# Performance work log

Measured on AMD Instinct MI355X. Metric: run time of the kernel, lower is better.

## Reference

```python
import jax, jax.numpy as jnp
import numpy as np

DIM = 768
HEADS = 12
HEAD_DIM = DIM // HEADS
HIDDEN = int(DIM * 4.0)
EPS = 1e-5


def layernorm(x, w, b):
    mu = jnp.mean(x, axis=-1, keepdims=True)
    var = jnp.var(x, axis=-1, keepdims=True)
    return (x - mu) * jax.lax.rsqrt(var + EPS) * w + b


def setup_inputs() -> dict:
    key = jax.random.key(0)
    ks = jax.random.split(key, 12)
    B, N = 4, 2048
    s = lambda fan_in: 1.0 / np.sqrt(fan_in)
    return {
        "x": jax.random.normal(ks[0], (B, N, DIM), dtype=jnp.float32),
        "qkv_w": jax.random.normal(ks[1], (3 * DIM, DIM), dtype=jnp.float32) * s(DIM),
        "proj_w": jax.random.normal(ks[2], (DIM, DIM), dtype=jnp.float32) * s(DIM),
        "proj_b": jnp.zeros((DIM,), dtype=jnp.float32),
        "norm1_w": jnp.ones((DIM,), dtype=jnp.float32),
        "norm1_b": jnp.zeros((DIM,), dtype=jnp.float32),
        "norm2_w": jnp.ones((DIM,), dtype=jnp.float32),
        "norm2_b": jnp.zeros((DIM,), dtype=jnp.float32),
        "fc1_w": jax.random.normal(ks[3], (HIDDEN, DIM), dtype=jnp.float32) * s(DIM),
        "fc1_b": jnp.zeros((HIDDEN,), dtype=jnp.float32),
        "fc2_w": jax.random.normal(ks[4], (DIM, HIDDEN), dtype=jnp.float32) * s(HIDDEN),
        "fc2_b": jnp.zeros((DIM,), dtype=jnp.float32),
    }


def reference(x, qkv_w, proj_w, proj_b, norm1_w, norm1_b, norm2_w, norm2_b,
              fc1_w, fc1_b, fc2_w, fc2_b):
    B, N, C = x.shape
    scale = HEAD_DIM ** -0.5
    shortcut = x
    h = layernorm(x, norm1_w, norm1_b)
    # qkv: [B, N, 3C] -> [3, B, H, N, Dh]
    qkv = (h @ qkv_w.T).reshape(B, N, 3, HEADS, HEAD_DIM)
    qkv = jnp.transpose(qkv, (2, 0, 3, 1, 4))
    q, k, v = qkv[0] * scale, qkv[1], qkv[2]
    attn = jnp.einsum("bhnd,bhmd->bhnm", q, k)
    attn = jax.nn.softmax(attn, axis=-1)
    out = jnp.einsum("bhnm,bhmd->bhnd", attn, v)
    out = jnp.transpose(out, (0, 2, 1, 3)).reshape(B, N, C)
    out = out @ proj_w.T + proj_b
    x = shortcut + out
    h2 = layernorm(x, norm2_w, norm2_b)
    mlp = jax.nn.gelu(h2 @ fc1_w.T + fc1_b, approximate=False) @ fc2_w.T + fc2_b
    return x + mlp
```

## Files before the change

### kernel.cpp

```cpp
#include <hip/hip_runtime.h>
#include <hip/hip_bf16.h>

#define SEQ   2048
#define NBAT  4
#define NH    12
#define HD    64
#define CDIM  768
#define HID   3072
#define NTOK  (SEQ*NBAT)

#define KS2 0.1803368801111244f

typedef __attribute__((ext_vector_type(8))) short short8;
typedef __attribute__((ext_vector_type(4))) float floatx4;

__device__ __forceinline__ float bf2f(unsigned short u) {
    union { unsigned int i; float f; } v; v.i = ((unsigned int)u) << 16; return v.f;
}
__device__ __forceinline__ unsigned short f2bf(float f) {
    union { float f; unsigned int i; } v; v.f = f;
    unsigned int i = v.i;
    return (unsigned short)((i + 0x7FFFu + ((i >> 16) & 1u)) >> 16);
}
__device__ __forceinline__ unsigned int fbits(float f) {
    union { float f; unsigned int i; } v; v.f = f; return v.i;
}
__device__ __forceinline__ float fast_exp2(float x) {
#if __has_builtin(__builtin_amdgcn_exp2f)
    return __builtin_amdgcn_exp2f(x);
#else
    return __expf(x * 0.69314718055994531f);
#endif
}
__device__ __forceinline__ float fast_rcp(float x) {
#if __has_builtin(__builtin_amdgcn_rcpf)
    return __builtin_amdgcn_rcpf(x);
#else
    return 1.f / x;
#endif
}
__device__ __forceinline__ float gelu_f(float v) {
    float u = 0.7978845608028654f * v * (1.f + 0.044715f * v * v);
    float e = fast_exp2(u * 2.885390081777927f);
    float th = 1.f - 2.f * fast_rcp(e + 1.f);
    return 0.5f * v * (1.f + th);
}
__device__ __forceinline__ void gload16(const unsigned short* g, unsigned short* l) {
    __builtin_amdgcn_global_load_lds(
        (const __attribute__((address_space(1))) unsigned int*)g,
        (__attribute__((address_space(3))) unsigned int*)l, 16, 0, 0);
}
__device__ __forceinline__ void pl32_swap(unsigned int& x, unsigned int& y) {
    asm("v_permlane32_swap_b32 %0, %1" : "+v"(x), "+v"(y));
}
__device__ __forceinline__ void pl16_swap(unsigned int& x, unsigned int& y) {
    asm("v_permlane16_swap_b32 %0, %1" : "+v"(x), "+v"(y));
}

__global__ __launch_bounds__(256) void cvt_all_kernel(
    const float* __restrict__ s0, const float* __restrict__ s1,
    const float* __restrict__ s2, const float* __restrict__ s3,
    unsigned short* __restrict__ d0, unsigned short* __restrict__ d1,
    unsigned short* __restrict__ d2, unsigned short* __restrict__ d3)
{
    int blk = blockIdx.x;
    const float* src; unsigned short* dst; int off;
    if (blk < 1728)      { src = s0; dst = d0; off = blk; }
    else if (blk < 2304) { src = s1; dst = d1; off = blk - 1728; }
    else if (blk < 4608) { src = s2; dst = d2; off = blk - 2304; }
    else                 { src = s3; dst = d3; off = blk - 4608; }
    int i = (off * 256 + threadIdx.x) * 4;
    float4 f = *(const float4*)(src + i);
    ushort4 o;
    o.x = f2bf(f.x); o.y = f2bf(f.y); o.z = f2bf(f.z); o.w = f2bf(f.w);
    *(ushort4*)(dst + i) = o;
}

__global__ __launch_bounds__(256) void ln_kernel(
    const float* __restrict__ x, const float* __restrict__ w,
    const float* __restrict__ b, unsigned short* __restrict__ y)
{
    int row  = blockIdx.x * 4 + (threadIdx.x >> 6);
    int lane = threadIdx.x & 63;
    const float4* xr = (const float4*)(x + (size_t)row * CDIM);
    float4 v[3];
    float s = 0.f, sq = 0.f;
#pragma unroll
    for (int i = 0; i < 3; i++) {
        float4 f = xr[lane + i * 64];
        v[i] = f;
        s  += (f.x + f.y) + (f.z + f.w);
        sq += (f.x * f.x + f.y * f.y) + (f.z * f.z + f.w * f.w);
    }
#pragma unroll
    for (int o = 32; o > 0; o >>= 1) {
        s  += __shfl_xor(s,  o, 64);
        sq += __shfl_xor(sq, o, 64);
    }
    float mean = s * (1.f / CDIM);
    float var  = sq * (1.f / CDIM) - mean * mean;
    float rstd = rsqrtf(var + 1e-5f);
    const float4* w4 = (const float4*)w;
    const float4* b4 = (const float4*)b;
    ushort4* y4 = (ushort4*)(y + (size_t)row * CDIM);
#pragma unroll
    for (int i = 0; i < 3; i++) {
        int c = lane + i * 64;
        float4 wf = w4[c], bf_ = b4[c];
        ushort4 o;
        o.x = f2bf((v[i].x - mean) * rstd * wf.x + bf_.x);
        o.y = f2bf((v[i].y - mean) * rstd * wf.y + bf_.y);
        o.z = f2bf((v[i].z - mean) * rstd * wf.z + bf_.z);
        o.w = f2bf((v[i].w - mean) * rstd * wf.w + bf_.w);
        y4[c] = o;
    }
}

#define BK 64

template<int ACT, int OUT32, int TM, int DBUF>
__global__ __launch_bounds__(256) void gemm_bt(
    const unsigned short* __restrict__ A, const unsigned short* __restrict__ W,
    const float* __restrict__ bias, const float* __restrict__ res,
    void* __restrict__ Cv, int M, int N, int K, int scol, float scale)
{
    constexpr int MT   = TM / 32;
    constexpr int ISSA = TM / 32;
    constexpr int NB   = DBUF ? 2 : 1;
    __shared__ __align__(16) unsigned short As[NB * TM * BK];
    __shared__ __align__(16) unsigned short Bs[NB * 128 * BK];
    int tid  = threadIdx.x;
    int wave = tid >> 6, lane = tid & 63;
    int wr = wave >> 1, wc = wave & 1;
    int quad = lane >> 4, l15 = lane & 15;
    int m0 = blockIdx.x * TM, n0 = blockIdx.y * 128;

    int r8 = lane >> 3;
    int kc = (lane & 7) ^ r8;
    const unsigned short* Ag = A + (size_t)(m0 + wave * (TM / 4) + r8) * K + kc * 8;
    const unsigned short* Wg = W + (size_t)(n0 + wave * 32 + r8) * K + kc * 8;
    unsigned short* AsW = As + wave * (TM / 4) * BK;
    unsigned short* BsW = Bs + wave * 32 * BK;

    floatx4 acc[MT][4];
    floatx4 fz = {0.f, 0.f, 0.f, 0.f};
#pragma unroll
    for (int i = 0; i < MT; i++)
#pragma unroll
        for (int j = 0; j < 4; j++) acc[i][j] = fz;

    int sw = l15 & 7;

    if constexpr (DBUF == 0) {
        for (int k0 = 0; k0 < K; k0 += BK) {
            __syncthreads();
#pragma unroll
            for (int j = 0; j < ISSA; j++)
                gload16(Ag + (size_t)(8 * j) * K + k0, AsW + j * 512);
#pragma unroll
            for (int j = 0; j < 4; j++)
                gload16(Wg + (size_t)(8 * j) * K + k0, BsW + j * 512);
            __syncthreads();

#pragma unroll
            for (int s = 0; s < 2; s++) {
                short8 af[MT], bfg[4];
                int ko = ((s * 4 + quad) ^ sw) * 8;
#pragma unroll
                for (int mt = 0; mt < MT; mt++)
                    af[mt] = *(const short8*)(As + (wr * (TM / 2) + mt * 16 + l15) * BK + ko);
#pragma unroll
                for (int nt = 0; nt < 4; nt++)
                    bfg[nt] = *(const short8*)(Bs + (wc * 64 + nt * 16 + l15) * BK + ko);
#pragma unroll
                for (int mt = 0; mt < MT; mt++)
#pragma unroll
                    for (int nt = 0; nt < 4; nt++)
                        acc[mt][nt] = __builtin_amdgcn_mfma_f32_16x16x32_bf16(
                            af[mt], bfg[nt], acc[mt][nt], 0, 0, 0);
            }
        }
    } else {
#pragma unroll
        for (int j = 0; j < ISSA; j++)
            gload16(Ag + (size_t)(8 * j) * K, AsW + j * 512);
#pragma unroll
        for (int j = 0; j < 4; j++)
            gload16(Wg + (size_t)(8 * j) * K, BsW + j * 512);
        int cur = 0;
        for (int k0 = 0; k0 < K; k0 += BK) {
            __syncthreads();
            if (k0 + BK < K) {
                int nb = cur ^ 1;
#pragma unroll
                for (int j = 0; j < ISSA; j++)
                    gload16(Ag + (size_t)(8 * j) * K + k0 + BK, AsW + nb * (TM * BK) + j * 512);
#pragma unroll
                for (int j = 0; j < 4; j++)
                    gload16(Wg + (size_t)(8 * j) * K + k0 + BK, BsW + nb * (128 * BK) + j * 512);
            }
            const unsigned short* Asb = As + cur * (TM * BK);
            const unsigned short* Bsb = Bs + cur * (128 * BK);
#pragma unroll
            for (int s = 0; s < 2; s++) {
                short8 af[MT], bfg[4];
                int ko = ((s * 4 + quad) ^ sw) * 8;
#pragma unroll
                for (int mt = 0; mt < MT; mt++)
                    af[mt] = *(const short8*)(Asb + (wr * (TM / 2) + mt * 16 + l15) * BK + ko);
#pragma unroll
                for (int nt = 0; nt < 4; nt++)
                    bfg[nt] = *(const short8*)(Bsb + (wc * 64 + nt * 16 + l15) * BK + ko);
#pragma unroll
                for (int mt = 0; mt < MT; mt++)
#pragma unroll
                    for (int nt = 0; nt < 4; nt++)
                        acc[mt][nt] = __builtin_amdgcn_mfma_f32_16x16x32_bf16(
                            af[mt], bfg[nt], acc[mt][nt], 0, 0, 0);
            }
            cur ^= 1;
        }
    }

#pragma unroll
    for (int mt = 0; mt < MT; mt++) {
#pragma unroll
        for (int nt = 0; nt < 4; nt++) {
            int col = n0 + wc * 64 + nt * 16 + l15;
            float bv = bias ? bias[col] : 0.f;
            float cs = (col < scol) ? scale : 1.f;
#pragma unroll
            for (int r = 0; r < 4; r++) {
                int row = m0 + wr * (TM / 2) + mt * 16 + quad * 4 + r;
                size_t idx = (size_t)row * N + col;
                float v = acc[mt][nt][r] + bv;
                if (res) v += res[idx];
                if (ACT == 1) v = gelu_f(v);
                v *= cs;
                if (OUT32) ((float*)Cv)[idx] = v;
                else       ((unsigned short*)Cv)[idx] = f2bf(v);
            }
        }
    }
}

__global__ __launch_bounds__(256, 4) void attn_kernel(
    const unsigned short* __restrict__ qkv, unsigned short* __restrict__ out)
{
    __shared__ __align__(16) unsigned short Ks[2][64 * 64];
    __shared__ __align__(16) unsigned short Vt[2][64 * 72];

    int tid  = threadIdx.x;
    int wave = tid >> 6, lane = tid & 63;
    int quad = lane >> 4, l15 = lane & 15;

    int f  = blockIdx.y * gridDim.x + blockIdx.x;
    int w_ = (f & 7) * 96 + (f >> 3);
    int qblk = w_ & 15;
    int bh   = w_ >> 4;
    int b  = bh / NH, h = bh % NH;
    size_t base = (size_t)b * SEQ * 2304 + h * 64;
    int qbase = qblk * 128 + wave * 32;

    short8 bq[2][2];
#pragma unroll
    for (int qh = 0; qh < 2; qh++)
#pragma unroll
        for (int kk = 0; kk < 2; kk++)
            bq[qh][kk] = *(const short8*)(qkv + base +
                (size_t)(qbase + qh * 16 + l15) * 2304 + kk * 32 + quad * 8);

    floatx4 o[2][4];
    floatx4 fz = {0.f, 0.f, 0.f, 0.f};
#pragma unroll
    for (int qh = 0; qh < 2; qh++)
#pragma unroll
        for (int dg = 0; dg < 4; dg++) o[qh][dg] = fz;
    float ls[2] = {0.f, 0.f};

    const unsigned short* kg = qkv + base + 768 +
        (size_t)(wave * 16 + (lane >> 3)) * 2304 + (((lane & 7) ^ ((lane >> 3) & 7)) * 8);
    const unsigned short* vptr = qkv + base + 1536;
    int vj  = tid & 31;
    int vd8 = wave * 16 + ((tid >> 5) & 1) * 8;
    int sw  = l15 & 7;

    gload16(kg, &Ks[0][wave * 1024]);
    gload16(kg + (size_t)8 * 2304, &Ks[0][wave * 1024 + 512]);
    {
        uint4 v0v = *(const uint4*)(vptr + (size_t)(2 * vj)     * 2304 + vd8);
        uint4 v1v = *(const uint4*)(vptr + (size_t)(2 * vj + 1) * 2304 + vd8);
        union { uint4 q; unsigned short u[8]; } u0, u1;
        u0.q = v0v; u1.q = v1v;
#pragma unroll
        for (int i = 0; i < 8; i++) {
            unsigned int w = (unsigned int)u0.u[i] | ((unsigned int)u1.u[i] << 16);
            *(unsigned int*)(&Vt[0][(vd8 + i) * 72 + 2 * vj]) = w;
        }
    }
    __syncthreads();

    for (int t = 0; t < SEQ / 64; t++) {
        int cur = t & 1, nxt = cur ^ 1;
        bool more = (t + 1 < SEQ / 64);
        uint4 v0v, v1v;
        if (more) {
            const unsigned short* kg2 = kg + (size_t)(t + 1) * 64 * 2304;
            gload16(kg2, &Ks[nxt][wave * 1024]);
            gload16(kg2 + (size_t)8 * 2304, &Ks[nxt][wave * 1024 + 512]);
            int kt = (t + 1) * 64;
            v0v = *(const uint4*)(vptr + (size_t)(kt + 2 * vj)     * 2304 + vd8);
            v1v = *(const uint4*)(vptr + (size_t)(kt + 2 * vj + 1) * 2304 + vd8);
        }

        floatx4 st[2][4];
        __builtin_amdgcn_s_setprio(1);
#pragma unroll
        for (int ts = 0; ts < 4; ts++) {
            short8 ak0 = *(const short8*)(&Ks[cur][(ts * 16 + l15) * 64 + (((0 * 4 + quad) ^ sw) * 8)]);
            short8 ak1 = *(const short8*)(&Ks[cur][(ts * 16 + l15) * 64 + (((1 * 4 + quad) ^ sw) * 8)]);
            floatx4 s0 = __builtin_amdgcn_mfma_f32_16x16x32_bf16(ak0, bq[0][0], fz, 0, 0, 0);
            s0 = __builtin_amdgcn_mfma_f32_16x16x32_bf16(ak1, bq[0][1], s0, 0, 0, 0);
            floatx4 s1 = __builtin_amdgcn_mfma_f32_16x16x32_bf16(ak0, bq[1][0], fz, 0, 0, 0);
            s1 = __builtin_amdgcn_mfma_f32_16x16x32_bf16(ak1, bq[1][1], s1, 0, 0, 0);
            st[0][ts] = s0; st[1][ts] = s1;
        }
        __builtin_amdgcn_s_setprio(0);

        unsigned int pw[2][4][2];
#pragma unroll
        for (int qh = 0; qh < 2; qh++) {
            float psum = 0.f;
#pragma unroll
            for (int ts = 0; ts < 4; ts++) {
                float p0 = fast_exp2(st[qh][ts][0]);
                float p1 = fast_exp2(st[qh][ts][1]);
                float p2 = fast_exp2(st[qh][ts][2]);
                float p3 = fast_exp2(st[qh][ts][3]);
                psum += (p0 + p1) + (p2 + p3);
                pw[qh][ts][0] = __builtin_amdgcn_perm(fbits(p1), fbits(p0), 0x07060302);
                pw[qh][ts][1] = __builtin_amdgcn_perm(fbits(p3), fbits(p2), 0x07060302);
            }
            ls[qh] += psum;
        }

#pragma unroll
        for (int hk = 0; hk < 2; hk++) {
            short8 bp[2];
#pragma unroll
            for (int qh = 0; qh < 2; qh++) {
                unsigned int x0 = pw[qh][2 * hk][0], y0 = pw[qh][2 * hk + 1][0];
                unsigned int x1 = pw[qh][2 * hk][1], y1 = pw[qh][2 * hk + 1][1];
                pl32_swap(x0, y0); pl16_swap(x0, y0);
                pl32_swap(x1, y1); pl16_swap(x1, y1);
                union { unsigned int u[4]; short8 s; } fu;
                fu.u[0] = x0; fu.u[1] = x1; fu.u[2] = y0; fu.u[3] = y1;
                bp[qh] = fu.s;
            }
            __builtin_amdgcn_s_setprio(1);
#pragma unroll
            for (int dg = 0; dg < 4; dg++) {
                short8 av = *(const short8*)(&Vt[cur][(dg * 16 + l15) * 72 + hk * 32 + quad * 8]);
                o[0][dg] = __builtin_amdgcn_mfma_f32_16x16x32_bf16(av, bp[0], o[0][dg], 0, 0, 0);
                o[1][dg] = __builtin_amdgcn_mfma_f32_16x16x32_bf16(av, bp[1], o[1][dg], 0, 0, 0);
            }
            __builtin_amdgcn_s_setprio(0);
        }

        if (more) {
            union { uint4 q; unsigned short u[8]; } u0, u1;
            u0.q = v0v; u1.q = v1v;
#pragma unroll
            for (int i = 0; i < 8; i++) {
                unsigned int w = (unsigned int)u0.u[i] | ((unsigned int)u1.u[i] << 16);
                *(unsigned int*)(&Vt[nxt][(vd8 + i) * 72 + 2 * vj]) = w;
            }
        }
        __syncthreads();
    }

#pragma unroll
    for (int qh = 0; qh < 2; qh++) {
        float l = ls[qh];
        l += __shfl_xor(l, 16, 64);
        l += __shfl_xor(l, 32, 64);
        float inv = 1.f / l;
        size_t orow = ((size_t)b * SEQ + qbase + qh * 16 + l15) * CDIM + h * 64;
#pragma unroll
        for (int dg = 0; dg < 4; dg++) {
            unsigned int u0 = (unsigned int)f2bf(o[qh][dg][0] * inv) | ((unsigned int)f2bf(o[qh][dg][1] * inv) << 16);
            unsigned int u1 = (unsigned int)f2bf(o[qh][dg][2] * inv) | ((unsigned int)f2bf(o[qh][dg][3] * inv) << 16);
            uint2 wv; wv.x = u0; wv.y = u1;
            *(uint2*)((unsigned short*)out + orow + dg * 16 + quad * 4) = wv;
        }
    }
}

extern "C" void kernel_launch(void* const* d_in, const int* in_sizes, int n_in,
                              void* d_out, int out_size, void* d_ws, size_t ws_size,
                              hipStream_t stream)
{
    const float* x      = (const float*)d_in[0];
    const float* qkv_w  = (const float*)d_in[1];
    const float* proj_w = (const float*)d_in[2];
    const float* proj_b = (const float*)d_in[3];
    const float* n1w    = (const float*)d_in[4];
    const float* n1b    = (const float*)d_in[5];
    const float* n2w    = (const float*)d_in[6];
    const float* n2b    = (const float*)d_in[7];
    const float* fc1w   = (const float*)d_in[8];
    const float* fc1b   = (const float*)d_in[9];
    const float* fc2w   = (const float*)d_in[10];
    const float* fc2b   = (const float*)d_in[11];
    float* out = (float*)d_out;

    unsigned short* ws = (unsigned short*)d_ws;
    unsigned short* wq = ws;
    unsigned short* wp = wq + 1769472;
    unsigned short* w1 = wp + 589824;
    unsigned short* w2 = w1 + 2359296;
    unsigned short* h    = w2 + 2359296;
    unsigned short* qkv  = h + 6291456;
    unsigned short* attn = qkv + 18874368;
    unsigned short* a    = qkv;

    dim3 blk(256);
    cvt_all_kernel<<<6912, blk, 0, stream>>>(qkv_w, proj_w, fc1w, fc2w, wq, wp, w1, w2);

    ln_kernel<<<NTOK / 4, blk, 0, stream>>>(x, n1w, n1b, h);
    gemm_bt<0, 0, 128, 0><<<dim3(NTOK / 128, 2304 / 128), blk, 0, stream>>>(
        h, wq, nullptr, nullptr, qkv, NTOK, 2304, 768, 768, KS2);
    attn_kernel<<<dim3(SEQ / 128, NBAT * NH), blk, 0, stream>>>(qkv, attn);
    gemm_bt<0, 1, 64, 1><<<dim3(NTOK / 64, 768 / 128), blk, 0, stream>>>(
        attn, wp, proj_b, x, out, NTOK, 768, 768, 0, 1.f);
    ln_kernel<<<NTOK / 4, blk, 0, stream>>>(out, n2w, n2b, h);
    gemm_bt<1, 0, 128, 0><<<dim3(NTOK / 128, 3072 / 128), blk, 0, stream>>>(
        h, w1, fc1b, nullptr, a, NTOK, 3072, 768, 0, 1.f);
    gemm_bt<0, 1, 64, 1><<<dim3(NTOK / 64, 768 / 128), blk, 0, stream>>>(
        a, w2, fc2b, out, out, NTOK, 768, 3072, 0, 1.f);
}
```

Before: 359.2 us.

## Split attention query block across eight waves of 16 rows each

After: 361.9 us, median of 2. No clear change (+0.7%).

```diff
diff --git a/kernel.cpp b/kernel.cpp
--- a/kernel.cpp
+++ b/kernel.cpp
@@ -244,7 +244,7 @@
     }
 }
 
-__global__ __launch_bounds__(256, 4) void attn_kernel(
+__global__ __launch_bounds__(512, 4) void attn_kernel(
     const unsigned short* __restrict__ qkv, unsigned short* __restrict__ out)
 {
     __shared__ __align__(16) unsigned short Ks[2][64 * 64];
@@ -260,34 +260,29 @@
     int bh   = w_ >> 4;
     int b  = bh / NH, h = bh % NH;
     size_t base = (size_t)b * SEQ * 2304 + h * 64;
-    int qbase = qblk * 128 + wave * 32;
-
-    short8 bq[2][2];
-#pragma unroll
-    for (int qh = 0; qh < 2; qh++)
-#pragma unroll
-        for (int kk = 0; kk < 2; kk++)
-            bq[qh][kk] = *(const short8*)(qkv + base +
-                (size_t)(qbase + qh * 16 + l15) * 2304 + kk * 32 + quad * 8);
-
-    floatx4 o[2][4];
+    int qbase = qblk * 128 + wave * 16;
+
+    short8 bq[2];
+#pragma unroll
+    for (int kk = 0; kk < 2; kk++)
+        bq[kk] = *(const short8*)(qkv + base +
+            (size_t)(qbase + l15) * 2304 + kk * 32 + quad * 8);
+
+    floatx4 o[4];
     floatx4 fz = {0.f, 0.f, 0.f, 0.f};
 #pragma unroll
-    for (int qh = 0; qh < 2; qh++)
-#pragma unroll
-        for (int dg = 0; dg < 4; dg++) o[qh][dg] = fz;
-    float ls[2] = {0.f, 0.f};
+    for (int dg = 0; dg < 4; dg++) o[dg] = fz;
+    float ls = 0.f;
 
     const unsigned short* kg = qkv + base + 768 +
-        (size_t)(wave * 16 + (lane >> 3)) * 2304 + (((lane & 7) ^ ((lane >> 3) & 7)) * 8);
+        (size_t)(wave * 8 + (lane >> 3)) * 2304 + (((lane & 7) ^ ((lane >> 3) & 7)) * 8);
     const unsigned short* vptr = qkv + base + 1536;
     int vj  = tid & 31;
     int vd8 = wave * 16 + ((tid >> 5) & 1) * 8;
     int sw  = l15 & 7;
 
-    gload16(kg, &Ks[0][wave * 1024]);
-    gload16(kg + (size_t)8 * 2304, &Ks[0][wave * 1024 + 512]);
-    {
+    gload16(kg, &Ks[0][wave * 512]);
+    if (wave < 4) {
         uint4 v0v = *(const uint4*)(vptr + (size_t)(2 * vj)     * 2304 + vd8);
         uint4 v1v = *(const uint4*)(vptr + (size_t)(2 * vj + 1) * 2304 + vd8);
         union { uint4 q; unsigned short u[8]; } u0, u1;
@@ -306,68 +301,61 @@
         uint4 v0v, v1v;
         if (more) {
             const unsigned short* kg2 = kg + (size_t)(t + 1) * 64 * 2304;
-            gload16(kg2, &Ks[nxt][wave * 1024]);
-            gload16(kg2 + (size_t)8 * 2304, &Ks[nxt][wave * 1024 + 512]);
-            int kt = (t + 1) * 64;
-            v0v = *(const uint4*)(vptr + (size_t)(kt + 2 * vj)     * 2304 + vd8);
-            v1v = *(const uint4*)(vptr + (size_t)(kt + 2 * vj + 1) * 2304 + vd8);
-        }
-
-        floatx4 st[2][4];
+            gload16(kg2, &Ks[nxt][wave * 512]);
+            if (wave < 4) {
+                int kt = (t + 1) * 64;
+                v0v = *(const uint4*)(vptr + (size_t)(kt + 2 * vj)     * 2304 + vd8);
+                v1v = *(const uint4*)(vptr + (size_t)(kt + 2 * vj + 1) * 2304 + vd8);
+            }
+        }
+
+        floatx4 st[4];
         __builtin_amdgcn_s_setprio(1);
 #pragma unroll
         for (int ts = 0; ts < 4; ts++) {
             short8 ak0 = *(const short8*)(&Ks[cur][(ts * 16 + l15) * 64 + (((0 * 4 + quad) ^ sw) * 8)]);
             short8 ak1 = *(const short8*)(&Ks[cur][(ts * 16 + l15) * 64 + (((1 * 4 + quad) ^ sw) * 8)]);
-            floatx4 s0 = __builtin_amdgcn_mfma_f32_16x16x32_bf16(ak0, bq[0][0], fz, 0, 0, 0);
-            s0 = __builtin_amdgcn_mfma_f32_16x16x32_bf16(ak1, bq[0][1], s0, 0, 0, 0);
-            floatx4 s1 = __builtin_amdgcn_mfma_f32_16x16x32_bf16(ak0, bq[1][0], fz, 0, 0, 0);
-            s1 = __builtin_amdgcn_mfma_f32_16x16x32_bf16(ak1, bq[1][1], s1, 0, 0, 0);
-            st[0][ts] = s0; st[1][ts] = s1;
+            floatx4 s0 = __builtin_amdgcn_mfma_f32_16x16x32_bf16(ak0, bq[0], fz, 0, 0, 0);
+            s0 = __builtin_amdgcn_mfma_f32_16x16x32_bf16(ak1, bq[1], s0, 0, 0, 0);
+            st[ts] = s0;
         }
         __builtin_amdgcn_s_setprio(0);
 
-        unsigned int pw[2][4][2];
-#pragma unroll
-        for (int qh = 0; qh < 2; qh++) {
+        unsigned int pw[4][2];
+        {
             float psum = 0.f;
 #pragma unroll
             for (int ts = 0; ts < 4; ts++) {
-                float p0 = fast_exp2(st[qh][ts][0]);
-                float p1 = fast_exp2(st[qh][ts][1]);
-                float p2 = fast_exp2(st[qh][ts][2]);
-                float p3 = fast_exp2(st[qh][ts][3]);
+                float p0 = fast_exp2(st[ts][0]);
+                float p1 = fast_exp2(st[ts][1]);
+                float p2 = fast_exp2(st[ts][2]);
+                float p3 = fast_exp2(st[ts][3]);
                 psum += (p0 + p1) + (p2 + p3);
-                pw[qh][ts][0] = __builtin_amdgcn_perm(fbits(p1), fbits(p0), 0x07060302);
-                pw[qh][ts][1] = __builtin_amdgcn_perm(fbits(p3), fbits(p2), 0x07060302);
-            }
-            ls[qh] += psum;
+                pw[ts][0] = __builtin_amdgcn_perm(fbits(p1), fbits(p0), 0x07060302);
+                pw[ts][1] = __builtin_amdgcn_perm(fbits(p3), fbits(p2), 0x07060302);
+            }
+            ls += psum;
         }
 
 #pragma unroll
         for (int hk = 0; hk < 2; hk++) {
-            short8 bp[2];
-#pragma unroll
-            for (int qh = 0; qh < 2; qh++) {
-                unsigned int x0 = pw[qh][2 * hk][0], y0 = pw[qh][2 * hk + 1][0];
-                unsigned int x1 = pw[qh][2 * hk][1], y1 = pw[qh][2 * hk + 1][1];
-                pl32_swap(x0, y0); pl16_swap(x0, y0);
-                pl32_swap(x1, y1); pl16_swap(x1, y1);
-                union { unsigned int u[4]; short8 s; } fu;
-                fu.u[0] = x0; fu.u[1] = x1; fu.u[2] = y0; fu.u[3] = y1;
-                bp[qh] = fu.s;
-            }
+            unsigned int x0 = pw[2 * hk][0], y0 = pw[2 * hk + 1][0];
+            unsigned int x1 = pw[2 * hk][1], y1 = pw[2 * hk + 1][1];
+            pl32_swap(x0, y0); pl16_swap(x0, y0);
+            pl32_swap(x1, y1); pl16_swap(x1, y1);
+            union { unsigned int u[4]; short8 s; } fu;
+            fu.u[0] = x0; fu.u[1] = x1; fu.u[2] = y0; fu.u[3] = y1;
+            short8 bp = fu.s;
             __builtin_amdgcn_s_setprio(1);
 #pragma unroll
             for (int dg = 0; dg < 4; dg++) {
                 short8 av = *(const short8*)(&Vt[cur][(dg * 16 + l15) * 72 + hk * 32 + quad * 8]);
-                o[0][dg] = __builtin_amdgcn_mfma_f32_16x16x32_bf16(av, bp[0], o[0][dg], 0, 0, 0);
-                o[1][dg] = __builtin_amdgcn_mfma_f32_16x16x32_bf16(av, bp[1], o[1][dg], 0, 0, 0);
+                o[dg] = __builtin_amdgcn_mfma_f32_16x16x32_bf16(av, bp, o[dg], 0, 0, 0);
             }
             __builtin_amdgcn_s_setprio(0);
         }
 
-        if (more) {
+        if (more && wave < 4) {
             union { uint4 q; unsigned short u[8]; } u0, u1;
             u0.q = v0v; u1.q = v1v;
 #pragma unroll
@@ -379,17 +367,16 @@
         __syncthreads();
     }
 
-#pragma unroll
-    for (int qh = 0; qh < 2; qh++) {
-        float l = ls[qh];
+    {
+        float l = ls;
         l += __shfl_xor(l, 16, 64);
         l += __shfl_xor(l, 32, 64);
         float inv = 1.f / l;
-        size_t orow = ((size_t)b * SEQ + qbase + qh * 16 + l15) * CDIM + h * 64;
+        size_t orow = ((size_t)b * SEQ + qbase + l15) * CDIM + h * 64;
 #pragma unroll
         for (int dg = 0; dg < 4; dg++) {
-            unsigned int u0 = (unsigned int)f2bf(o[qh][dg][0] * inv) | ((unsigned int)f2bf(o[qh][dg][1] * inv) << 16);
-            unsigned int u1 = (unsigned int)f2bf(o[qh][dg][2] * inv) | ((unsigned int)f2bf(o[qh][dg][3] * inv) << 16);
+            unsigned int u0 = (unsigned int)f2bf(o[dg][0] * inv) | ((unsigned int)f2bf(o[dg][1] * inv) << 16);
+            unsigned int u1 = (unsigned int)f2bf(o[dg][2] * inv) | ((unsigned int)f2bf(o[dg][3] * inv) << 16);
             uint2 wv; wv.x = u0; wv.y = u1;
             *(uint2*)((unsigned short*)out + orow + dg * 16 + quad * 4) = wv;
         }
@@ -430,7 +417,7 @@
     ln_kernel<<<NTOK / 4, blk, 0, stream>>>(x, n1w, n1b, h);
     gemm_bt<0, 0, 128, 0><<<dim3(NTOK / 128, 2304 / 128), blk, 0, stream>>>(
         h, wq, nullptr, nullptr, qkv, NTOK, 2304, 768, 768, KS2);
-    attn_kernel<<<dim3(SEQ / 128, NBAT * NH), blk, 0, stream>>>(qkv, attn);
+    attn_kernel<<<dim3(SEQ / 128, NBAT * NH), dim3(512), 0, stream>>>(qkv, attn);
     gemm_bt<0, 1, 64, 1><<<dim3(NTOK / 64, 768 / 128), blk, 0, stream>>>(
         attn, wp, proj_b, x, out, NTOK, 768, 768, 0, 1.f);
     ln_kernel<<<NTOK / 4, blk, 0, stream>>>(out, n2w, n2b, h);
```
